# Kernel optimization log

Hardware: AMD Instinct MI355X
Metric: run time of the kernel (lower is better)

Reference implementation:

```python
import jax, jax.numpy as jnp
import numpy as np

B, IN, H = 8192, 1024, 1024


def setup_inputs() -> dict:
    key = jax.random.key(0)
    ks = jax.random.split(key, 6)
    s = 1.0 / np.sqrt(H)
    return {
        "incoming": jax.random.normal(ks[0], (B, IN), dtype=jnp.float32),
        "state": jax.random.normal(ks[1], (2, B, H), dtype=jnp.float32),
        "Wx": jax.random.normal(ks[2], (4 * H, IN), dtype=jnp.float32) * s,
        "bx": jax.random.normal(ks[3], (4 * H,), dtype=jnp.float32) * s,
        "Wh": jax.random.normal(ks[4], (4 * H, H), dtype=jnp.float32) * s,
        "bh": jax.random.normal(ks[5], (4 * H,), dtype=jnp.float32) * s,
    }


def reference(incoming, state, Wx, bx, Wh, bh):
    # Fused form of 8 Linear layers: gates stacked in (i, f, g, o) order.
    h_prev, c_prev = state[0], state[1]
    gates = (jnp.einsum('bi,gi->bg', incoming, Wx) + bx
             + jnp.einsum('bh,gh->bg', h_prev, Wh) + bh)  # [B, 4H]
    i_g, f_g, g_g, o_g = jnp.split(gates, 4, axis=-1)
    i = jax.nn.sigmoid(i_g)
    f = jax.nn.sigmoid(f_g)
    g = jnp.tanh(g_g)
    o = jax.nn.sigmoid(o_g)
    new_c = f * c_prev + i * g
    new_h = o * jnp.tanh(new_c)
    # output == new_h; return stacked (new_h, new_c) as [2, B, H]
    return jnp.stack([new_h, new_c])
```

## Files before the change

### kernel.cpp

```cpp
#include <hip/hip_runtime.h>
#include <hip/hip_bf16.h>


#define B_DIM 8192
#define H_DIM 1024
#define BH (8192 * 1024)
#define K2 2048

typedef __attribute__((ext_vector_type(4))) float f32x4;
typedef __attribute__((ext_vector_type(8))) __bf16 bf16x8;
typedef __attribute__((ext_vector_type(8))) unsigned short ushort8;

static __device__ __forceinline__ unsigned short f2bf(float f) {
    return __builtin_bit_cast(unsigned short, (__bf16)f);
}
static __device__ __forceinline__ float sigf(float x) {
    return 1.0f / (1.0f + __expf(-x));
}
static __device__ __forceinline__ float tanhft(float x) {
    float e = __expf(2.0f * x);
    return (e - 1.0f) / (e + 1.0f);
}
static __device__ __forceinline__ void gload16(const void* g, void* l) {
    __builtin_amdgcn_global_load_lds(
        (const __attribute__((address_space(1))) unsigned int*)g,
        (__attribute__((address_space(3))) unsigned int*)l, 16, 0, 0);
}
static __device__ __forceinline__ ushort8 cvt8(const float* src) {
    const float4 u = ((const float4*)src)[0];
    const float4 v = ((const float4*)src)[1];
    ushort8 o;
    o[0] = f2bf(u.x); o[1] = f2bf(u.y); o[2] = f2bf(u.z); o[3] = f2bf(u.w);
    o[4] = f2bf(v.x); o[5] = f2bf(v.y); o[6] = f2bf(v.z); o[7] = f2bf(v.w);
    return o;
}

__global__ __launch_bounds__(256) void conv_kernel(
    const float* __restrict__ x, const float* __restrict__ h,
    const float* __restrict__ Wx, const float* __restrict__ Wh,
    unsigned short* __restrict__ A, unsigned short* __restrict__ W)
{
    const int bidx = blockIdx.x;
    if (bidx < 8192) {
        const int id = bidx * 256 + threadIdx.x;
        const int base = id * 8;
        const int b = base >> 11;
        const int k = base & 2047;
        const float* src = (k < 1024) ? (x + (size_t)b * 1024 + k)
                                      : (h + (size_t)b * 1024 + (k - 1024));
        *(ushort8*)(A + base) = cvt8(src);
    } else {
        const int id = (bidx - 8192) * 256 + threadIdx.x;
        const int base = id * 8;
        const int n = base >> 11;
        const int k = base & 2047;
        const int jb = n >> 8, wn = (n >> 6) & 3, g = (n >> 4) & 3, jj = n & 15;
        const int srow = (g << 10) + (jb << 6) + (wn << 4) + jj;
        const float* src = (k < 1024) ? (Wx + (size_t)srow * 1024 + k)
                                      : (Wh + (size_t)srow * 1024 + (k - 1024));
        *(ushort8*)(W + base) = cvt8(src);
    }
}

__global__ __launch_bounds__(512, 2) void lstm_gemm8(
    const unsigned short* __restrict__ Abf, const unsigned short* __restrict__ Wbf,
    const float* __restrict__ bx, const float* __restrict__ bh,
    const float* __restrict__ cprev, float* __restrict__ out)
{
    extern __shared__ unsigned short lds[];

    const int tid = threadIdx.x;
    const int lane = tid & 63;
    const int wv = tid >> 6;
    const int wm = wv >> 2;
    const int wn = wv & 3;
    const int q = lane >> 4, c = lane & 15;

    const int bid = blockIdx.x;
    const int xcd = bid & 7;
    const int idx = bid >> 3;
    const int jb  = xcd * 2 + (idx & 1);
    const int bb  = idx >> 1;
    const int b0 = bb * 256;

    const unsigned short* Ab = Abf + (size_t)b0 * K2;
    const unsigned short* Wb = Wbf + (size_t)(jb * 256) * K2;

    const int srow = tid >> 2;
    const int sk8g = (tid & 3) ^ ((tid >> 3) & 3);
    const size_t ss0 = (size_t)srow * K2 + (size_t)sk8g * 8;
    const unsigned sdst = (unsigned)(tid & 448) * 8;

    const int cq = ((q ^ ((c >> 1) & 3)) << 3);
    const unsigned aoff = (unsigned)(wm * 128 + c) * 32 + cq;
    const unsigned boff = 16384u + (unsigned)(wn * 64 + c) * 32 + cq;

    f32x4 acc[8][4];
#pragma unroll
    for (int m = 0; m < 8; ++m)
#pragma unroll
        for (int g = 0; g < 4; ++g) acc[m][g] = f32x4{0.f, 0.f, 0.f, 0.f};

    bf16x8 av[4], bv[4];

#define STAGE(TP, T, ISB, KS) do {                                             \
    const unsigned short* _s = (ISB) ? Wb : Ab;                                \
    const size_t _o = ss0 + (size_t)((T) & 31) * 64 + (KS) * 32;               \
    const unsigned _d = ((TP) << 15) | ((ISB) << 14) | ((KS) << 13);           \
    gload16(_s + _o, &lds[_d + sdst]);                                         \
    gload16(_s + (size_t)128 * K2 + _o, &lds[_d + 4096u + sdst]);              \
} while (0)

#define LOADA(BUF, KS, MH) do {                                                \
    const unsigned short* _p = lds + (BUF) * 32768 + (KS) * 8192 + aoff + (MH) * 2048; \
    av[0] = *(const bf16x8*)(_p);                                              \
    av[1] = *(const bf16x8*)(_p + 512);                                        \
    av[2] = *(const bf16x8*)(_p + 1024);                                       \
    av[3] = *(const bf16x8*)(_p + 1536);                                       \
} while (0)

#define LOADB(BUF, KS) do {                                                    \
    const unsigned short* _p = lds + (BUF) * 32768 + (KS) * 8192 + boff;       \
    bv[0] = *(const bf16x8*)(_p);                                              \
    bv[1] = *(const bf16x8*)(_p + 512);                                        \
    bv[2] = *(const bf16x8*)(_p + 1024);                                       \
    bv[3] = *(const bf16x8*)(_p + 1536);                                       \
} while (0)

#define MFMA16(MH) do {                                                        \
    __builtin_amdgcn_s_setprio(1);                                             \
    _Pragma("unroll")                                                          \
    for (int _i = 0; _i < 4; ++_i)                                             \
        _Pragma("unroll")                                                      \
        for (int _g = 0; _g < 4; ++_g)                                         \
            acc[(MH) * 4 + _i][_g] = __builtin_amdgcn_mfma_f32_16x16x32_bf16(  \
                av[_i], bv[_g], acc[(MH) * 4 + _i][_g], 0, 0, 0);              \
    __builtin_amdgcn_s_setprio(0);                                             \
} while (0)

#define BAR_SOFT() __builtin_amdgcn_s_barrier()
#define BAR_FENCE() asm volatile("s_barrier" ::: "memory")
#define WAIT_LGKM() asm volatile("s_waitcnt lgkmcnt(0)" ::: "memory")
#define WAIT_VM8() asm volatile("s_waitcnt vmcnt(8)" ::: "memory")

#define PH0(BUF, KS, STP, ST, SB, SK) do {                                     \
    LOADA(BUF, KS, 0);                                                         \
    LOADB(BUF, KS);                                                            \
    STAGE(STP, ST, SB, SK);                                                    \
    BAR_SOFT();                                                                \
    WAIT_LGKM();                                                               \
    MFMA16(0);                                                                 \
    BAR_FENCE();                                                               \
} while (0)

#define PH1(BUF, KS, STP, ST, SB, SK) do {                                     \
    LOADA(BUF, KS, 1);                                                         \
    STAGE(STP, ST, SB, SK);                                                    \
    BAR_SOFT();                                                                \
    WAIT_LGKM();                                                               \
    MFMA16(1);                                                                 \
    WAIT_VM8();                                                                \
    BAR_FENCE();                                                               \
} while (0)

    STAGE(0, 0, 0, 0); STAGE(0, 0, 1, 0); STAGE(0, 0, 0, 1); STAGE(0, 0, 1, 1);
    STAGE(1, 1, 0, 0); STAGE(1, 1, 1, 0);
    WAIT_VM8();
    BAR_FENCE();

    for (int u = 0; u < 32; u += 2) {
        PH0(0, 0, 1, u + 1, 0, 1);
        PH1(0, 0, 1, u + 1, 1, 1);
        PH0(0, 1, 0, u + 2, 0, 0);
        PH1(0, 1, 0, u + 2, 1, 0);
        PH0(1, 0, 0, u + 2, 0, 1);
        PH1(1, 0, 0, u + 2, 1, 1);
        PH0(1, 1, 1, u + 3, 0, 0);
        PH1(1, 1, 1, u + 3, 1, 0);
    }

#undef PH0
#undef PH1
#undef STAGE
#undef LOADA
#undef LOADB
#undef MFMA16

    const int j = jb * 64 + wn * 16 + c;
    const float bI = bx[j] + bh[j];
    const float bF = bx[1024 + j] + bh[1024 + j];
    const float bG = bx[2048 + j] + bh[2048 + j];
    const float bO = bx[3072 + j] + bh[3072 + j];
#pragma unroll
    for (int mt = 0; mt < 8; ++mt) {
#pragma unroll
        for (int rr = 0; rr < 4; ++rr) {
            const int row = b0 + wm * 128 + mt * 16 + q * 4 + rr;
            const size_t off = (size_t)row * 1024 + j;
            const float iv = sigf(acc[mt][0][rr] + bI);
            const float fv = sigf(acc[mt][1][rr] + bF);
            const float gv = tanhft(acc[mt][2][rr] + bG);
            const float ov = sigf(acc[mt][3][rr] + bO);
            const float cp = cprev[off];
            const float nc = fv * cp + iv * gv;
            out[off] = ov * tanhft(nc);
            out[BH + off] = nc;
        }
    }
}

__global__ __launch_bounds__(256) void lstm_fallback(
    const float* __restrict__ incoming, const float* __restrict__ state,
    const float* __restrict__ Wx, const float* __restrict__ bx,
    const float* __restrict__ Wh, const float* __restrict__ bh,
    float* __restrict__ out)
{
    __shared__ unsigned short lA[128 * 64];
    __shared__ unsigned short lW[128 * 64];
    const int t = threadIdx.x;
    const int lane = t & 63;
    const int wv = t >> 6;
    const int q = lane >> 4;
    const int c = lane & 15;
    const int j0 = blockIdx.x * 32;
    const int b0 = blockIdx.y * 128;
    const float* hprev = state;
    const float* cprev = state + (size_t)BH;

    f32x4 acc[2][8];
#pragma unroll
    for (int mt = 0; mt < 2; ++mt)
#pragma unroll
        for (int nt = 0; nt < 8; ++nt)
            acc[mt][nt] = f32x4{0.f, 0.f, 0.f, 0.f};

    const int sr = t >> 3;
    const int sk8 = t & 7;

    for (int it = 0; it < 32; ++it) {
        const bool first = (it < 16);
        const float* As = first ? incoming : hprev;
        const float* Ws = first ? Wx : Wh;
        const int kk = first ? it * 64 : it * 64 - 1024;
#pragma unroll
        for (int i = 0; i < 4; ++i) {
            const int r = i * 32 + sr;
            *(ushort8*)&lA[r * 64 + ((sk8 ^ (r & 7)) * 8)] =
                cvt8(As + (size_t)(b0 + r) * 1024 + kk + sk8 * 8);
        }
#pragma unroll
        for (int i = 0; i < 4; ++i) {
            const int n = i * 32 + sr;
            const int grow = ((n >> 5) << 10) + j0 + (n & 31);
            *(ushort8*)&lW[n * 64 + ((sk8 ^ (n & 7)) * 8)] =
                cvt8(Ws + (size_t)grow * 1024 + kk + sk8 * 8);
        }
        __syncthreads();
#pragma unroll
        for (int ks = 0; ks < 2; ++ks) {
            const int k8a = ks * 4 + q;
            bf16x8 av[2], bv[8];
#pragma unroll
            for (int mt = 0; mt < 2; ++mt) {
                const int r = wv * 32 + mt * 16 + c;
                av[mt] = *(const bf16x8*)&lA[r * 64 + ((k8a ^ (r & 7)) * 8)];
            }
#pragma unroll
            for (int nt = 0; nt < 8; ++nt) {
                const int n = nt * 16 + c;
                bv[nt] = *(const bf16x8*)&lW[n * 64 + ((k8a ^ (n & 7)) * 8)];
            }
#pragma unroll
            for (int mt = 0; mt < 2; ++mt)
#pragma unroll
                for (int nt = 0; nt < 8; ++nt)
                    acc[mt][nt] = __builtin_amdgcn_mfma_f32_16x16x32_bf16(
                        av[mt], bv[nt], acc[mt][nt], 0, 0, 0);
        }
        __syncthreads();
    }

    const int b0r = b0 + wv * 32;
#pragma unroll
    for (int jt = 0; jt < 2; ++jt) {
        const int j = j0 + jt * 16 + c;
        const float bI = bx[j] + bh[j];
        const float bF = bx[1024 + j] + bh[1024 + j];
        const float bG = bx[2048 + j] + bh[2048 + j];
        const float bO = bx[3072 + j] + bh[3072 + j];
#pragma unroll
        for (int mt = 0; mt < 2; ++mt) {
#pragma unroll
            for (int rr = 0; rr < 4; ++rr) {
                const int row = b0r + mt * 16 + q * 4 + rr;
                const size_t off = (size_t)row * 1024 + j;
                const float iv = sigf(acc[mt][0 + jt][rr] + bI);
                const float fv = sigf(acc[mt][2 + jt][rr] + bF);
                const float gv = tanhft(acc[mt][4 + jt][rr] + bG);
                const float ov = sigf(acc[mt][6 + jt][rr] + bO);
                const float cp = cprev[off];
                const float nc = fv * cp + iv * gv;
                out[off] = ov * tanhft(nc);
                out[BH + off] = nc;
            }
        }
    }
}

extern "C" void kernel_launch(void* const* d_in, const int* in_sizes, int n_in,
                              void* d_out, int out_size, void* d_ws, size_t ws_size,
                              hipStream_t stream) {
    const float* incoming = (const float*)d_in[0];
    const float* state    = (const float*)d_in[1];
    const float* Wx       = (const float*)d_in[2];
    const float* bx       = (const float*)d_in[3];
    const float* Wh       = (const float*)d_in[4];
    const float* bh       = (const float*)d_in[5];
    float* out = (float*)d_out;

    const float* hprev = state;
    const float* cprev = state + (size_t)BH;

    const size_t A_bytes = (size_t)B_DIM * K2 * 2;
    const size_t W_bytes = (size_t)4 * H_DIM * K2 * 2;

    if (ws_size >= A_bytes + W_bytes) {
        unsigned short* Abf = (unsigned short*)d_ws;
        unsigned short* Wbf = (unsigned short*)((char*)d_ws + A_bytes);
        conv_kernel<<<dim3(12288), dim3(256), 0, stream>>>(
            incoming, hprev, Wx, Wh, Abf, Wbf);
        (void)hipFuncSetAttribute((const void*)lstm_gemm8,
                                  hipFuncAttributeMaxDynamicSharedMemorySize, 131072);
        lstm_gemm8<<<dim3(512), dim3(512), 131072, stream>>>(
            Abf, Wbf, bx, bh, cprev, out);
    } else {
        dim3 grid(H_DIM / 32, B_DIM / 128);
        lstm_fallback<<<grid, dim3(256), 0, stream>>>(
            incoming, state, Wx, bx, Wh, bh, out);
    }
}
```

Measured before the change: 164.7 us.

## Double-buffer LDS fragment registers to overlap ds_reads with MFMA

Splits the A and B operand registers into two alternating sets so the LDS reads for the next sub-step are issued before the current MFMA block runs, instead of waiting on lgkmcnt before each block. The soft barrier and lgkm waits are dropped, and the vmcnt wait moves to 6 in alternating phases, so synchronisation changes throughout the pipeline. This uses more VGPRs and relies on compiler-inserted waits for the LDS data, which could hurt occupancy or correctness if a barrier ordering is off. Prefetching across the final iteration also reads buffer 0 after the loop ends.

```diff
diff --git a/kernel.cpp b/kernel.cpp
--- a/kernel.cpp
+++ b/kernel.cpp
@@ -101,7 +101,7 @@
 #pragma unroll
         for (int g = 0; g < 4; ++g) acc[m][g] = f32x4{0.f, 0.f, 0.f, 0.f};
 
-    bf16x8 av[4], bv[4];
+    bf16x8 avE[4], avO[4], bvA[4], bvB[4];
 
 #define STAGE(TP, T, ISB, KS) do {                                             \
     const unsigned short* _s = (ISB) ? Wb : Ab;                                \
@@ -111,79 +111,66 @@
     gload16(_s + (size_t)128 * K2 + _o, &lds[_d + 4096u + sdst]);              \
 } while (0)
 
-#define LOADA(BUF, KS, MH) do {                                                \
+#define RDA(DST, BUF, KS, MH) do {                                             \
     const unsigned short* _p = lds + (BUF) * 32768 + (KS) * 8192 + aoff + (MH) * 2048; \
-    av[0] = *(const bf16x8*)(_p);                                              \
-    av[1] = *(const bf16x8*)(_p + 512);                                        \
-    av[2] = *(const bf16x8*)(_p + 1024);                                       \
-    av[3] = *(const bf16x8*)(_p + 1536);                                       \
+    DST[0] = *(const bf16x8*)(_p);                                             \
+    DST[1] = *(const bf16x8*)(_p + 512);                                       \
+    DST[2] = *(const bf16x8*)(_p + 1024);                                      \
+    DST[3] = *(const bf16x8*)(_p + 1536);                                      \
 } while (0)
 
-#define LOADB(BUF, KS) do {                                                    \
+#define RDB(DST, BUF, KS) do {                                                 \
     const unsigned short* _p = lds + (BUF) * 32768 + (KS) * 8192 + boff;       \
-    bv[0] = *(const bf16x8*)(_p);                                              \
-    bv[1] = *(const bf16x8*)(_p + 512);                                        \
-    bv[2] = *(const bf16x8*)(_p + 1024);                                       \
-    bv[3] = *(const bf16x8*)(_p + 1536);                                       \
+    DST[0] = *(const bf16x8*)(_p);                                             \
+    DST[1] = *(const bf16x8*)(_p + 512);                                       \
+    DST[2] = *(const bf16x8*)(_p + 1024);                                      \
+    DST[3] = *(const bf16x8*)(_p + 1536);                                      \
 } while (0)
 
-#define MFMA16(MH) do {                                                        \
+#define MFMA16(AV, MH, BV) do {                                                \
     __builtin_amdgcn_s_setprio(1);                                             \
     _Pragma("unroll")                                                          \
     for (int _i = 0; _i < 4; ++_i)                                             \
         _Pragma("unroll")                                                      \
         for (int _g = 0; _g < 4; ++_g)                                         \
             acc[(MH) * 4 + _i][_g] = __builtin_amdgcn_mfma_f32_16x16x32_bf16(  \
-                av[_i], bv[_g], acc[(MH) * 4 + _i][_g], 0, 0, 0);              \
+                AV[_i], BV[_g], acc[(MH) * 4 + _i][_g], 0, 0, 0);              \
     __builtin_amdgcn_s_setprio(0);                                             \
 } while (0)
 
-#define BAR_SOFT() __builtin_amdgcn_s_barrier()
-#define BAR_FENCE() asm volatile("s_barrier" ::: "memory")
-#define WAIT_LGKM() asm volatile("s_waitcnt lgkmcnt(0)" ::: "memory")
-#define WAIT_VM8() asm volatile("s_waitcnt vmcnt(8)" ::: "memory")
-
-#define PH0(BUF, KS, STP, ST, SB, SK) do {                                     \
-    LOADA(BUF, KS, 0);                                                         \
-    LOADB(BUF, KS);                                                            \
-    STAGE(STP, ST, SB, SK);                                                    \
-    BAR_SOFT();                                                                \
-    WAIT_LGKM();                                                               \
-    MFMA16(0);                                                                 \
-    BAR_FENCE();                                                               \
-} while (0)
-
-#define PH1(BUF, KS, STP, ST, SB, SK) do {                                     \
-    LOADA(BUF, KS, 1);                                                         \
-    STAGE(STP, ST, SB, SK);                                                    \
-    BAR_SOFT();                                                                \
-    WAIT_LGKM();                                                               \
-    MFMA16(1);                                                                 \
-    WAIT_VM8();                                                                \
-    BAR_FENCE();                                                               \
-} while (0)
+#define BAR()  asm volatile("s_barrier" ::: "memory")
+#define WVM6() asm volatile("s_waitcnt vmcnt(6)" ::: "memory")
+#define WVM8() asm volatile("s_waitcnt vmcnt(8)" ::: "memory")
 
     STAGE(0, 0, 0, 0); STAGE(0, 0, 1, 0); STAGE(0, 0, 0, 1); STAGE(0, 0, 1, 1);
     STAGE(1, 1, 0, 0); STAGE(1, 1, 1, 0);
-    WAIT_VM8();
-    BAR_FENCE();
+    WVM8();
+    BAR();
+    RDA(avE, 0, 0, 0);
+    RDB(bvA, 0, 0);
 
     for (int u = 0; u < 32; u += 2) {
-        PH0(0, 0, 1, u + 1, 0, 1);
-        PH1(0, 0, 1, u + 1, 1, 1);
-        PH0(0, 1, 0, u + 2, 0, 0);
-        PH1(0, 1, 0, u + 2, 1, 0);
-        PH0(1, 0, 0, u + 2, 0, 1);
-        PH1(1, 0, 0, u + 2, 1, 1);
-        PH0(1, 1, 1, u + 3, 0, 0);
-        PH1(1, 1, 1, u + 3, 1, 0);
-    }
-
-#undef PH0
-#undef PH1
+        RDA(avO, 0, 0, 1); STAGE(1, u + 1, 0, 1);
+        MFMA16(avE, 0, bvA); WVM6(); BAR();
+        RDA(avE, 0, 1, 0); RDB(bvB, 0, 1); STAGE(1, u + 1, 1, 1);
+        MFMA16(avO, 1, bvA); BAR();
+        RDA(avO, 0, 1, 1); STAGE(0, u + 2, 0, 0);
+        MFMA16(avE, 0, bvB); WVM6(); BAR();
+        RDA(avE, 1, 0, 0); RDB(bvA, 1, 0); STAGE(0, u + 2, 1, 0);
+        MFMA16(avO, 1, bvB); BAR();
+        RDA(avO, 1, 0, 1); STAGE(0, u + 2, 0, 1);
+        MFMA16(avE, 0, bvA); WVM6(); BAR();
+        RDA(avE, 1, 1, 0); RDB(bvB, 1, 1); STAGE(0, u + 2, 1, 1);
+        MFMA16(avO, 1, bvA); BAR();
+        RDA(avO, 1, 1, 1); STAGE(1, u + 3, 0, 0);
+        MFMA16(avE, 0, bvB); WVM6(); BAR();
+        RDA(avE, 0, 0, 0); RDB(bvA, 0, 0); STAGE(1, u + 3, 1, 0);
+        MFMA16(avO, 1, bvB); BAR();
+    }
+
 #undef STAGE
-#undef LOADA
-#undef LOADB
+#undef RDA
+#undef RDB
 #undef MFMA16
 
     const int j = jb * 64 + wn * 16 + c;
```

After: 162.4 us. Within noise of the previous version (-1.4%).
